# Kernel tuning notes

Hardware: AMD Instinct MI355X
Metric: run time of the kernel (lower is better)

The kernel has to match this reference:

```python
import jax, jax.numpy as jnp
import numpy as np

B, N, C, H, W = 256, 50000, 3, 32, 32


def setup_inputs() -> dict:
    key = jax.random.key(0)
    k1, k2, k3 = jax.random.split(key, 3)
    inp = jax.random.normal(k1, (B, C, H, W), dtype=jnp.float32)
    train_data = jax.random.normal(k2, (N, C, H, W), dtype=jnp.float32)
    # per-query noise levels in a realistic diffusion range
    sigma = jax.random.uniform(k3, (B,), dtype=jnp.float32) * 1.5 + 0.5
    return {"input": inp, "sigma": sigma, "train_data": train_data}


def reference(input, sigma, train_data):
    """Karras optimal denoiser:
    D(x, sigma) = sum_i y_i * Gau(x; y_i, sigma^2 I) / sum_i Gau(x; y_i, sigma^2 I).
    The Gaussian normalization constant (sigma*sqrt(2*pi))^D cancels in the ratio,
    so this is exactly softmax over -0.5*||x - y_i||^2 / sigma^2 (same math as the
    per-dim product of densities in the original, computed stably in log space).
    """
    b = input.shape[0]
    x = input.reshape(b, -1)                      # [B, D]
    y = train_data.reshape(train_data.shape[0], -1)  # [N, D]
    x2 = jnp.sum(x * x, axis=1, keepdims=True)    # [B, 1]
    y2 = jnp.sum(y * y, axis=1)                   # [N]
    # pairwise squared distances via GEMM: [B, N]
    sqdist = x2 + y2[None, :] - 2.0 * (x @ y.T)
    logw = -0.5 * sqdist / (sigma[:, None] ** 2)  # [B, N]
    w = jax.nn.softmax(logw, axis=1)              # normalized Gaussian weights
    out = w @ y                                   # [B, D] weighted average
    return out.reshape(input.shape)
```

## Files before the change

kernel.cpp:

```cpp
#include <hip/hip_runtime.h>
#include <hip/hip_bf16.h>
#include <type_traits>

#define BQ   256
#define NTR  50000
#define DD   3072
#define NSP  50048
#define NBLK 782
#define CAP  4096
#define DELTA 18.0f

typedef __fp16 f16;
typedef __fp16 f16x2 __attribute__((ext_vector_type(2)));
typedef __fp16 f16x8 __attribute__((ext_vector_type(8)));
typedef float  f32x4 __attribute__((ext_vector_type(4)));

__global__ __launch_bounds__(256) void kx(const float* __restrict__ x, f16* __restrict__ xp) {
    const int t = blockIdx.x * 256 + threadIdx.x;
    const int g = t >> 8, r = t & 255;
    const f32x4* src = (const f32x4*)(x + (size_t)r * DD + (g << 3));
    f32x4 a = src[0], b = src[1];
    union { f16x2 h2[4]; f16x8 h8; } u;
    u.h2[0] = __builtin_amdgcn_cvt_pkrtz(a[0], a[1]);
    u.h2[1] = __builtin_amdgcn_cvt_pkrtz(a[2], a[3]);
    u.h2[2] = __builtin_amdgcn_cvt_pkrtz(b[0], b[1]);
    u.h2[3] = __builtin_amdgcn_cvt_pkrtz(b[2], b[3]);
    ((f16x8*)xp)[t] = u.h8;
}

__global__ __launch_bounds__(512, 4) void kqk(
    const f16* __restrict__ xp, const float* __restrict__ y,
    f16* __restrict__ S, float* __restrict__ pmax) {
    __shared__ char Bs[2][8192];

    const int tid = threadIdx.x;
    const int blk = blockIdx.x;
    const int n0  = blk * 64;

    const int ry   = tid >> 3;
    const int kp   = (tid & 7) << 3;
    const int yrow = n0 + ry;
    const bool yval = yrow < NTR;
    const float* ybase = y + (size_t)yrow * DD + kp;
    const int bo = ry * 128 + ((((tid & 7) << 4)) ^ ((ry & 7) << 4));

    const int w = tid >> 6, l = tid & 63;
    const int l15 = l & 15, lg = l >> 4;

    f32x4 acc[2][4] = {};
    float y2a = 0.f;
    f32x4 p0, p1, q0, q1;

    auto loady = [&](f32x4& a0, f32x4& a1, int ks) {
        if (yval) {
            const f32x4* pp = (const f32x4*)(ybase + (ks << 6));
            a0 = pp[0]; a1 = pp[1];
        } else { a0 = 0.f; a1 = 0.f; }
    };
    auto cvtw = [&](f32x4& a0, f32x4& a1, int buf) {
        y2a += a0[0]*a0[0] + a0[1]*a0[1] + a0[2]*a0[2] + a0[3]*a0[3]
             + a1[0]*a1[0] + a1[1]*a1[1] + a1[2]*a1[2] + a1[3]*a1[3];
        union { f16x2 h2[4]; f16x8 h8; } u;
        u.h2[0] = __builtin_amdgcn_cvt_pkrtz(a0[0], a0[1]);
        u.h2[1] = __builtin_amdgcn_cvt_pkrtz(a0[2], a0[3]);
        u.h2[2] = __builtin_amdgcn_cvt_pkrtz(a1[0], a1[1]);
        u.h2[3] = __builtin_amdgcn_cvt_pkrtz(a1[2], a1[3]);
        *(f16x8*)(&Bs[buf][bo]) = u.h8;
    };

    loady(p0, p1, 0);
    loady(q0, q1, 1);
    cvtw(p0, p1, 0);
    asm volatile("s_waitcnt lgkmcnt(0)" ::: "memory");
    __builtin_amdgcn_s_barrier();

    const f16x8* ap = (const f16x8*)xp;
    const int arow = (w << 5) + l15;

    auto iter = [&](int ks, auto curC,
                    f32x4& s0, f32x4& s1,
                    f32x4& t0, f32x4& t1) {
        constexpr int cur = decltype(curC)::value;
        f16x8 af[2][2];
        #pragma unroll
        for (int kk = 0; kk < 2; ++kk)
            #pragma unroll
            for (int fm = 0; fm < 2; ++fm)
                af[kk][fm] = ap[(size_t)((ks << 3) + (kk << 2) + lg) * 256 + arow + (fm << 4)];
        if (ks + 2 < 48) loady(s0, s1, ks + 2);
        f16x8 bf[2][4];
        #pragma unroll
        for (int kk = 0; kk < 2; ++kk)
            #pragma unroll
            for (int fn = 0; fn < 4; ++fn) {
                int r = (fn << 4) + l15;
                bf[kk][fn] = *(const f16x8*)(&Bs[cur][r * 128 + (((kk << 6) + (lg << 4)) ^ ((r & 7) << 4))]);
            }
        #pragma unroll
        for (int kk = 0; kk < 2; ++kk)
            #pragma unroll
            for (int fm = 0; fm < 2; ++fm)
                #pragma unroll
                for (int fn = 0; fn < 4; ++fn)
                    acc[fm][fn] = __builtin_amdgcn_mfma_f32_16x16x32_f16(af[kk][fm], bf[kk][fn], acc[fm][fn], 0, 0, 0);
        if (ks + 1 < 48) cvtw(t0, t1, cur ^ 1);
        asm volatile("s_waitcnt lgkmcnt(0)" ::: "memory");
        __builtin_amdgcn_s_barrier();
    };

    for (int ks2 = 0; ks2 < 48; ks2 += 2) {
        iter(ks2,     std::integral_constant<int,0>{}, p0, p1, q0, q1);
        iter(ks2 + 1, std::integral_constant<int,1>{}, q0, q1, p0, p1);
    }

    float* lys = (float*)&Bs[0][0];
    y2a += __shfl_xor(y2a, 1, 64);
    y2a += __shfl_xor(y2a, 2, 64);
    y2a += __shfl_xor(y2a, 4, 64);
    if ((tid & 7) == 0) lys[ry] = y2a;
    __syncthreads();
    float ly2[4];
    #pragma unroll
    for (int fn = 0; fn < 4; ++fn) ly2[fn] = 0.5f * lys[(fn << 4) + l15];
    #pragma unroll
    for (int fm = 0; fm < 2; ++fm) {
        #pragma unroll
        for (int j = 0; j < 4; ++j) {
            float rm = -3.4e38f;
            #pragma unroll
            for (int fn = 0; fn < 4; ++fn) {
                int col = n0 + (fn << 4) + l15;
                float sc = acc[fm][fn][j] - ly2[fn];
                rm = (col < NTR) ? fmaxf(rm, sc) : rm;
            }
            #pragma unroll
            for (int off = 1; off < 16; off <<= 1) rm = fmaxf(rm, __shfl_xor(rm, off, 64));
            if (l15 == 0)
                pmax[(size_t)((w << 5) + (fm << 4) + (lg << 2) + j) * NBLK + blk] = rm;
        }
    }
    #pragma unroll
    for (int fm = 0; fm < 2; ++fm) {
        int row0 = (w << 5) + (fm << 4) + (lg << 2);
        #pragma unroll
        for (int fn = 0; fn < 4; ++fn) {
            int col = n0 + (fn << 4) + l15;
            f16* sp = S + (size_t)row0 * NSP + col;
            sp[0]               = (f16)(acc[fm][fn][0] - ly2[fn]);
            sp[NSP]             = (f16)(acc[fm][fn][1] - ly2[fn]);
            sp[2 * (size_t)NSP] = (f16)(acc[fm][fn][2] - ly2[fn]);
            sp[3 * (size_t)NSP] = (f16)(acc[fm][fn][3] - ly2[fn]);
        }
    }
}

__global__ __launch_bounds__(512) void ksp(
    const float* __restrict__ x, const float* __restrict__ y,
    const f16* __restrict__ S, const float* __restrict__ pmax,
    const float* __restrict__ sig, float* __restrict__ out) {
    __shared__ float xs[DD];
    __shared__ unsigned ci[CAP];
    __shared__ unsigned scnt;
    __shared__ float red[8];
    __shared__ float om[8], ol[8];
    __shared__ float sumv[DD];
    const int b = blockIdx.x, tid = threadIdx.x;
    const float s2 = sig[b] * sig[b];
    const float isc = -0.5f / s2;
    const int w = tid >> 6, l = tid & 63;

    if (tid == 0) scnt = 0;
    for (int i = tid; i < DD; i += 512) xs[i] = x[(size_t)b * DD + i];
    const float* pm = pmax + (size_t)b * NBLK;
    float mx = -3.4e38f;
    for (int i = tid; i < NBLK; i += 512) mx = fmaxf(mx, pm[i]);
    #pragma unroll
    for (int o = 1; o < 64; o <<= 1) mx = fmaxf(mx, __shfl_xor(mx, o, 64));
    if (l == 0) red[w] = mx;
    __syncthreads();
    mx = red[0];
    #pragma unroll
    for (int ww = 1; ww < 8; ++ww) mx = fmaxf(mx, red[ww]);
    const float thr = mx - DELTA * s2 - 2.0f;

    const f16x8* row = (const f16x8*)(S + (size_t)b * NSP);
    for (int i = tid; i < 6256; i += 512) {
        f16x8 v = row[i];
        #pragma unroll
        for (int j = 0; j < 8; ++j) {
            int idx = (i << 3) + j;
            if ((float)v[j] >= thr && idx < NTR) {
                unsigned p = atomicAdd(&scnt, 1u);
                if (p < CAP) ci[p] = (unsigned)idx;
            }
        }
    }
    __syncthreads();
    const int c = (int)(scnt < (unsigned)CAP ? scnt : (unsigned)CAP);

    const f32x4* xr = (const f32x4*)xs;
    f32x4 o[12] = {};
    float m = -3.4e38f, ll = 0.f;
    f32x4 A[12], Bv[12];

    auto LD = [&](f32x4* dst, int i) {
        const f32x4* yr = (const f32x4*)(y + (size_t)ci[i] * DD);
        #pragma unroll
        for (int j = 0; j < 12; ++j) dst[j] = yr[(j << 6) + l];
    };
    auto PROC = [&](f32x4* src) {
        float d2 = 0.f;
        #pragma unroll
        for (int j = 0; j < 12; ++j) {
            f32x4 xv = xr[(j << 6) + l];
            float a0 = xv[0]-src[j][0], a1 = xv[1]-src[j][1],
                  a2 = xv[2]-src[j][2], a3 = xv[3]-src[j][3];
            d2 += a0*a0 + a1*a1 + a2*a2 + a3*a3;
        }
        #pragma unroll
        for (int off = 1; off < 64; off <<= 1) d2 += __shfl_xor(d2, off, 64);
        float s = d2 * isc;
        float mn = fmaxf(m, s);
        float f = __expf(m - mn);
        float wi = __expf(s - mn);
        #pragma unroll
        for (int j = 0; j < 12; ++j) o[j] = o[j] * f + wi * src[j];
        ll = ll * f + wi;
        m = mn;
    };

    int i = w;
    if (i < c) LD(A, i);
    for (; i < c; i += 16) {
        int i2 = i + 8;
        if (i2 < c) LD(Bv, i2);
        PROC(A);
        if (i2 < c) {
            if (i + 16 < c) LD(A, i + 16);
            PROC(Bv);
        }
    }
    om[w] = m; ol[w] = ll;
    __syncthreads();
    float M = om[0];
    #pragma unroll
    for (int ww = 1; ww < 8; ++ww) M = fmaxf(M, om[ww]);
    float Ls = 0.f;
    #pragma unroll
    for (int ww = 0; ww < 8; ++ww) Ls += ol[ww] * __expf(om[ww] - M);
    const float fw = __expf(m - M);
    f32x4* sv = (f32x4*)sumv;
    if (w == 0) {
        #pragma unroll
        for (int j = 0; j < 12; ++j) sv[(j << 6) + l] = o[j] * fw;
    }
    __syncthreads();
    for (int ww = 1; ww < 8; ++ww) {
        if (w == ww) {
            #pragma unroll
            for (int j = 0; j < 12; ++j) sv[(j << 6) + l] += o[j] * fw;
        }
        __syncthreads();
    }
    const float inv = 1.f / Ls;
    f32x4* od = (f32x4*)(out + (size_t)b * DD);
    for (int t = tid; t < 768; t += 512) od[t] = sv[t] * inv;
}

extern "C" void kernel_launch(void* const* d_in, const int* in_sizes, int n_in,
                              void* d_out, int out_size, void* d_ws, size_t ws_size,
                              hipStream_t stream) {
    const float* x   = (const float*)d_in[0];
    const float* sig = (const float*)d_in[1];
    const float* y   = (const float*)d_in[2];
    float* out = (float*)d_out;
    char* ws = (char*)d_ws;
    f16*   xp   = (f16*)(ws);
    float* pmax = (float*)(ws + 1572864);
    f16*   S    = (f16*)(ws + 2373632);

    kx  <<<384, 256, 0, stream>>>(x, xp);
    kqk <<<NBLK, 512, 0, stream>>>(xp, y, S, pmax);
    ksp <<<256, 512, 0, stream>>>(x, y, S, pmax, sig, out);
}
```

Before: 245.9 us.

## Remap QK blocks per XCD and widen coalesced train-data row loads

Block indices are remapped so that each XCD handles a contiguous range of training rows, improving L2 locality on the multi-die GPU. The global load pattern for the fp32 training tile also changes: 16 threads now cover one row in 16-byte pieces, two rows per thread, where before 8 threads loaded 32 contiguous bytes each. This gives a wider contiguous span per row per instruction. The exchange is twice as many smaller 8-byte LDS writes and a wider shuffle reduction for y².

Result: no change. 243.7 us, median of 2 (-0.9%).

```diff
diff --git a/kernel.cpp b/kernel.cpp
--- a/kernel.cpp
+++ b/kernel.cpp
@@ -12,6 +12,7 @@
 
 typedef __fp16 f16;
 typedef __fp16 f16x2 __attribute__((ext_vector_type(2)));
+typedef __fp16 f16x4 __attribute__((ext_vector_type(4)));
 typedef __fp16 f16x8 __attribute__((ext_vector_type(8)));
 typedef float  f32x4 __attribute__((ext_vector_type(4)));
 
@@ -34,38 +35,42 @@
     __shared__ char Bs[2][8192];
 
     const int tid = threadIdx.x;
-    const int blk = blockIdx.x;
+    const int orig = blockIdx.x;
+    const int xcd = orig & 7, cidx = orig >> 3;
+    const int blk = (xcd < 6 ? xcd * 98 : 588 + (xcd - 6) * 97) + cidx;
     const int n0  = blk * 64;
 
-    const int ry   = tid >> 3;
-    const int kp   = (tid & 7) << 3;
-    const int yrow = n0 + ry;
-    const bool yval = yrow < NTR;
-    const float* ybase = y + (size_t)yrow * DD + kp;
-    const int bo = ry * 128 + ((((tid & 7) << 4)) ^ ((ry & 7) << 4));
+    const int ry0 = tid >> 4;
+    const int kc  = tid & 15;
+    const int yr0 = n0 + ry0, yr1 = yr0 + 32;
+    const bool yv0 = yr0 < NTR, yv1 = yr1 < NTR;
+    const float* yb0 = y + (size_t)yr0 * DD + (kc << 2);
+    const float* yb1 = y + (size_t)yr1 * DD + (kc << 2);
+    const int swz = (ry0 & 7) << 4;
+    const int bo0 = ry0 * 128        + (((((kc >> 1) << 4)) ^ swz) | ((kc & 1) << 3));
+    const int bo1 = (ry0 + 32) * 128 + (((((kc >> 1) << 4)) ^ swz) | ((kc & 1) << 3));
 
     const int w = tid >> 6, l = tid & 63;
     const int l15 = l & 15, lg = l >> 4;
 
     f32x4 acc[2][4] = {};
-    float y2a = 0.f;
+    float y2a0 = 0.f, y2a1 = 0.f;
     f32x4 p0, p1, q0, q1;
 
     auto loady = [&](f32x4& a0, f32x4& a1, int ks) {
-        if (yval) {
-            const f32x4* pp = (const f32x4*)(ybase + (ks << 6));
-            a0 = pp[0]; a1 = pp[1];
-        } else { a0 = 0.f; a1 = 0.f; }
+        a0 = yv0 ? *(const f32x4*)(yb0 + (ks << 6)) : f32x4(0.f);
+        a1 = yv1 ? *(const f32x4*)(yb1 + (ks << 6)) : f32x4(0.f);
     };
     auto cvtw = [&](f32x4& a0, f32x4& a1, int buf) {
-        y2a += a0[0]*a0[0] + a0[1]*a0[1] + a0[2]*a0[2] + a0[3]*a0[3]
-             + a1[0]*a1[0] + a1[1]*a1[1] + a1[2]*a1[2] + a1[3]*a1[3];
-        union { f16x2 h2[4]; f16x8 h8; } u;
-        u.h2[0] = __builtin_amdgcn_cvt_pkrtz(a0[0], a0[1]);
-        u.h2[1] = __builtin_amdgcn_cvt_pkrtz(a0[2], a0[3]);
-        u.h2[2] = __builtin_amdgcn_cvt_pkrtz(a1[0], a1[1]);
-        u.h2[3] = __builtin_amdgcn_cvt_pkrtz(a1[2], a1[3]);
-        *(f16x8*)(&Bs[buf][bo]) = u.h8;
+        y2a0 += a0[0]*a0[0] + a0[1]*a0[1] + a0[2]*a0[2] + a0[3]*a0[3];
+        y2a1 += a1[0]*a1[0] + a1[1]*a1[1] + a1[2]*a1[2] + a1[3]*a1[3];
+        union { f16x2 h2[2]; f16x4 h4; } u0, u1;
+        u0.h2[0] = __builtin_amdgcn_cvt_pkrtz(a0[0], a0[1]);
+        u0.h2[1] = __builtin_amdgcn_cvt_pkrtz(a0[2], a0[3]);
+        u1.h2[0] = __builtin_amdgcn_cvt_pkrtz(a1[0], a1[1]);
+        u1.h2[1] = __builtin_amdgcn_cvt_pkrtz(a1[2], a1[3]);
+        *(f16x4*)(&Bs[buf][bo0]) = u0.h4;
+        *(f16x4*)(&Bs[buf][bo1]) = u1.h4;
     };
 
     loady(p0, p1, 0);
@@ -114,10 +119,12 @@
     }
 
     float* lys = (float*)&Bs[0][0];
-    y2a += __shfl_xor(y2a, 1, 64);
-    y2a += __shfl_xor(y2a, 2, 64);
-    y2a += __shfl_xor(y2a, 4, 64);
-    if ((tid & 7) == 0) lys[ry] = y2a;
+    #pragma unroll
+    for (int off = 1; off < 16; off <<= 1) {
+        y2a0 += __shfl_xor(y2a0, off, 64);
+        y2a1 += __shfl_xor(y2a1, off, 64);
+    }
+    if ((tid & 15) == 0) { lys[ry0] = y2a0; lys[ry0 + 32] = y2a1; }
     __syncthreads();
     float ly2[4];
     #pragma unroll
```
